# Optimization experiments

Measured on AMD Instinct MI355X. Metric: run time of the kernel, lower is better.

The kernel has to match this reference:

```python
import jax, jax.numpy as jnp
import numpy as np

B, L, D, H, DH, DI, NL, V = 1, 2048, 1024, 16, 64, 4096, 12, 32000
EPS = 1e-5  # torch LayerNorm default eps
SCALE = 1.0 / DH ** 0.5


def _ln(x):
    # LayerNorm with elementwise_affine=False
    m = jnp.mean(x, axis=-1, keepdims=True)
    va = jnp.var(x, axis=-1, keepdims=True)
    return (x - m) / jnp.sqrt(va + EPS)


def setup_inputs() -> dict:
    key = jax.random.key(0)
    ks = jax.random.split(key, 12)
    s = 0.02
    return {
        "X": jax.random.randint(ks[0], (B, L), 0, V),
        "Y": jax.random.randint(ks[1], (B, L), 0, V),
        "emb": jax.random.normal(ks[2], (V, D), jnp.float32) * s,
        "u": jax.random.normal(ks[3], (H, DH), jnp.float32) * s,
        "v": jax.random.normal(ks[4], (H, DH), jnp.float32) * s,
        "Wqkv": jax.random.normal(ks[5], (NL, 3 * H * DH, D), jnp.float32) * s,
        "Wpe": jax.random.normal(ks[6], (NL, H * DH, D), jnp.float32) * s,
        "Wout": jax.random.normal(ks[7], (NL, D, H * DH), jnp.float32) * s,
        "W1": jax.random.normal(ks[8], (NL, DI, D), jnp.float32) * s,
        "b1": jnp.zeros((NL, DI), jnp.float32),
        "W2": jax.random.normal(ks[9], (NL, D, DI), jnp.float32) * s,
        "b2": jnp.zeros((NL, D), jnp.float32),
        "Wc": jax.random.normal(ks[10], (V, D), jnp.float32) * s,
        "bc": jnp.zeros((V,), jnp.float32),
    }


def _forward(X, emb, u, v, Wqkv, Wpe, Wout, W1, b1, W2, b2, Wc, bc):
    q_len = X.shape[1]
    k_len = q_len  # mems=None -> m_len=0
    h = emb[X]  # (B, L, D); d_embedding == d_model so no projection

    # sinusoidal relative position embedding over descending positions
    pos = jnp.arange(k_len - 1, -1, -1, dtype=h.dtype)
    inv_freq = 1.0 / (10000.0 ** (jnp.arange(0, D, 2, dtype=h.dtype) / D))
    pp = pos[:, None] * inv_freq[None, :]              # (k, D/2)
    pe = jnp.concatenate([jnp.sin(pp), jnp.cos(pp)], axis=1)[None]  # (1, k, D)

    # causal mask: triu(ones, diagonal=1 + m_len), m_len=0; True = masked
    mask = jnp.triu(jnp.ones((q_len, k_len), bool), k=1)

    def layer(hid, params):
        wqkv, wpe, wout, w1, bb1, w2, bb2 = params
        qkv = hid @ wqkv.T                              # (B, q, 3HD)
        Q, K, Vv = jnp.split(qkv, 3, axis=-1)
        Q = Q.reshape(B, q_len, H, DH)
        K = K.reshape(B, k_len, H, DH)
        Vv = Vv.reshape(B, k_len, H, DH)
        r = (pe @ wpe.T).reshape(B, k_len, H, DH)       # requires B == 1
        AC = jnp.einsum('bqhd,bkhd->bhqk', Q + u, K)
        # NOTE: original code calls relative_shift(BD) but DISCARDS the result,
        # so BD is used unshifted — we reproduce that faithfully.
        BD = jnp.einsum('bqhd,bkhd->bhqk', Q + v, r)
        score = (AC + BD) * SCALE
        score = jnp.where(mask[None, None], -jnp.inf, score)
        prob = jax.nn.softmax(score, axis=-1)
        av = jnp.einsum('bhqk,bkhd->bqhd', prob, Vv).reshape(B, q_len, H * DH)
        hid = _ln(hid + av @ wout.T)                    # post-norm attention
        ff = jax.nn.relu(hid @ w1.T + bb1) @ w2.T + bb2
        hid = _ln(hid + ff)                             # post-norm FFN
        return hid, None

    h, _ = jax.lax.scan(layer, h, (Wqkv, Wpe, Wout, W1, b1, W2, b2))
    logits = h @ Wc.T + bc                              # (B, L, V)
    return logits.reshape(B * q_len, V)


def reference(X, Y, emb, u, v, Wqkv, Wpe, Wout, W1, b1, W2, b2, Wc, bc):
    # Y only determines y_len; here y_len == q_len so the full hidden is used.
    return _forward(X, emb, u, v, Wqkv, Wpe, Wout, W1, b1, W2, b2, Wc, bc)
```

## Files before the change

### kernel.cpp

```cpp
#include <hip/hip_runtime.h>
#include <hip/hip_bf16.h>

#define L_ 2048
#define D_ 1024
#define H_ 16
#define DH_ 64
#define DI_ 4096
#define NL_ 12
#define V_ 32000
#define EPS_ 1e-5f
#define SCALE_ 0.125f
#define LOG2E_ 1.44269504f
#define KBLK 64

typedef __attribute__((ext_vector_type(8))) short short8;
typedef __attribute__((ext_vector_type(4))) float f32x4;
typedef __hip_bfloat16 bf16;

__device__ __forceinline__ void gload_lds16(const void* g, void* l) {
  __builtin_amdgcn_global_load_lds((const __attribute__((address_space(1))) void*)g,
                                   (__attribute__((address_space(3))) void*)l, 16, 0, 0);
}

__global__ __launch_bounds__(512)
void gemm256(const bf16* __restrict__ A, const bf16* __restrict__ B,
             float* __restrict__ C, const float* __restrict__ bias,
             int lda, int ldb, int ldc, int K)
{
  __shared__ __align__(16) bf16 As[2][256 * 64];
  __shared__ __align__(16) bf16 Bs[2][256 * 64];

  const int gx = gridDim.x;
  const int nwg = gx * gridDim.y;
  const int orig = blockIdx.x + gx * blockIdx.y;
  const int qq = nwg >> 3, rr = nwg & 7;
  const int xcd = orig & 7, sidx = orig >> 3;
  const int lin = (xcd < rr ? xcd * (qq + 1) : rr * (qq + 1) + (xcd - rr) * qq) + sidx;
  const int m0 = (lin % gx) * 256;
  const int n0 = (lin / gx) * 256;

  const int t = threadIdx.x;
  const int lane = t & 63, w = t >> 6;
  const int wm = w >> 2, wn = w & 3;
  const int rl = lane & 15, hi = lane >> 4;

  int srow[4], skb[4];
#pragma unroll
  for (int r = 0; r < 4; ++r) {
    int o = r * 8192 + t * 16;
    int s = o ^ (((o >> 9) & 1) << 5);
    srow[r] = s >> 7;
    skb[r] = s & 127;
  }

  auto stage = [&](int c, int kt) {
    const int k0 = kt * 64;
#pragma unroll
    for (int r = 0; r < 4; ++r)
      gload_lds16((const char*)A + ((size_t)(m0 + srow[r]) * lda + k0) * 2 + skb[r],
                  (char*)As[c] + r * 8192 + w * 1024);
#pragma unroll
    for (int r = 0; r < 4; ++r)
      gload_lds16((const char*)B + ((size_t)(n0 + srow[r]) * ldb + k0) * 2 + skb[r],
                  (char*)Bs[c] + r * 8192 + w * 1024);
  };

  f32x4 acc[8][4];
#pragma unroll
  for (int i = 0; i < 8; ++i)
#pragma unroll
    for (int j = 0; j < 4; ++j) acc[i][j] = (f32x4){0.f, 0.f, 0.f, 0.f};

  const int NT = K >> 6;
  stage(0, 0);
  stage(1, 1);
  asm volatile("s_waitcnt vmcnt(8)" ::: "memory");
  __builtin_amdgcn_s_barrier();
  asm volatile("" ::: "memory");

  int cur = 0;
  for (int kt = 0; kt < NT; ++kt) {
    short8 b[4][2];
#pragma unroll
    for (int nf = 0; nf < 4; ++nf)
#pragma unroll
      for (int ks = 0; ks < 2; ++ks) {
        int l = ((wn * 64 + nf * 16 + rl) << 7) + ks * 64 + hi * 16;
        b[nf][ks] = *(const short8*)((char*)Bs[cur] + (l ^ (((l >> 9) & 1) << 5)));
      }
#pragma unroll
    for (int p = 0; p < 4; ++p) {
      short8 a[2][2];
#pragma unroll
      for (int i = 0; i < 2; ++i)
#pragma unroll
        for (int ks = 0; ks < 2; ++ks) {
          int l = ((wm * 128 + (2 * p + i) * 16 + rl) << 7) + ks * 64 + hi * 16;
          a[i][ks] = *(const short8*)((char*)As[cur] + (l ^ (((l >> 9) & 1) << 5)));
        }
      __builtin_amdgcn_s_setprio(1);
#pragma unroll
      for (int i = 0; i < 2; ++i)
#pragma unroll
        for (int nf = 0; nf < 4; ++nf) {
          acc[2 * p + i][nf] = __builtin_amdgcn_mfma_f32_16x16x32_bf16(a[i][0], b[nf][0], acc[2 * p + i][nf], 0, 0, 0);
          acc[2 * p + i][nf] = __builtin_amdgcn_mfma_f32_16x16x32_bf16(a[i][1], b[nf][1], acc[2 * p + i][nf], 0, 0, 0);
        }
      __builtin_amdgcn_s_setprio(0);
      __builtin_amdgcn_sched_barrier(0);
    }
    __builtin_amdgcn_s_barrier();
    asm volatile("" ::: "memory");
    if (kt + 2 < NT) stage(cur, kt + 2);
    if (kt + 1 < NT) {
      if (kt + 2 < NT) asm volatile("s_waitcnt vmcnt(8)" ::: "memory");
      else             asm volatile("s_waitcnt vmcnt(0)" ::: "memory");
      __builtin_amdgcn_s_barrier();
      asm volatile("" ::: "memory");
    }
    cur ^= 1;
  }

#pragma unroll
  for (int mf = 0; mf < 8; ++mf) {
#pragma unroll
    for (int nf = 0; nf < 4; ++nf) {
#pragma unroll
      for (int j = 0; j < 4; ++j) {
        const int m = m0 + wm * 128 + mf * 16 + hi * 4 + j;
        const int n = n0 + wn * 64 + nf * 16 + rl;
        C[(size_t)m * ldc + n] = acc[mf][nf][j] + bias[n];
      }
    }
  }
}

template<int EPI>
__global__ __launch_bounds__(512)
void gemm256x128(const bf16* __restrict__ A, const bf16* __restrict__ B,
                 void* __restrict__ C, const float* __restrict__ bias,
                 int lda, int ldb, int ldc, int Kc, long long Cstride)
{
  __shared__ __align__(16) bf16 As[2][256 * 64];
  __shared__ __align__(16) bf16 Bs[2][128 * 64];

  const int gx = gridDim.x;
  const int nwg = gx * gridDim.y;
  const int orig = blockIdx.x + gx * blockIdx.y;
  const int qq = nwg >> 3, rr = nwg & 7;
  const int xcd = orig & 7, sidx = orig >> 3;
  const int lin = (xcd < rr ? xcd * (qq + 1) : rr * (qq + 1) + (xcd - rr) * qq) + sidx;
  const int m0 = (lin % gx) * 256;
  const int n0 = (lin / gx) * 128;

  const int kbeg = blockIdx.z * Kc;
  const size_t czoff = (size_t)blockIdx.z * (size_t)Cstride;

  const int t = threadIdx.x;
  const int lane = t & 63, w = t >> 6;
  const int wm = w >> 1, wn = w & 1;
  const int rl = lane & 15, hi = lane >> 4;

  int srow[4], skb[4];
#pragma unroll
  for (int r = 0; r < 4; ++r) {
    int o = r * 8192 + t * 16;
    int s = o ^ (((o >> 9) & 1) << 5);
    srow[r] = s >> 7;
    skb[r] = s & 127;
  }

  auto stage = [&](int c, int kt) {
    const int k0 = kbeg + kt * 64;
#pragma unroll
    for (int r = 0; r < 4; ++r)
      gload_lds16((const char*)A + ((size_t)(m0 + srow[r]) * lda + k0) * 2 + skb[r],
                  (char*)As[c] + r * 8192 + w * 1024);
#pragma unroll
    for (int r = 0; r < 2; ++r)
      gload_lds16((const char*)B + ((size_t)(n0 + srow[r]) * ldb + k0) * 2 + skb[r],
                  (char*)Bs[c] + r * 8192 + w * 1024);
  };

  f32x4 acc[4][4];
#pragma unroll
  for (int i = 0; i < 4; ++i)
#pragma unroll
    for (int j = 0; j < 4; ++j) acc[i][j] = (f32x4){0.f, 0.f, 0.f, 0.f};

  const int NT = Kc >> 6;
  stage(0, 0);
  stage(1, 1);
  asm volatile("s_waitcnt vmcnt(6)" ::: "memory");
  __builtin_amdgcn_s_barrier();
  asm volatile("" ::: "memory");

  int cur = 0;
  for (int kt = 0; kt < NT; ++kt) {
    short8 b[4][2];
#pragma unroll
    for (int nf = 0; nf < 4; ++nf)
#pragma unroll
      for (int ks = 0; ks < 2; ++ks) {
        int l = ((wn * 64 + nf * 16 + rl) << 7) + ks * 64 + hi * 16;
        b[nf][ks] = *(const short8*)((char*)Bs[cur] + (l ^ (((l >> 9) & 1) << 5)));
      }
#pragma unroll
    for (int p = 0; p < 4; ++p) {
      short8 a[2];
#pragma unroll
      for (int ks = 0; ks < 2; ++ks) {
        int l = ((wm * 64 + p * 16 + rl) << 7) + ks * 64 + hi * 16;
        a[ks] = *(const short8*)((char*)As[cur] + (l ^ (((l >> 9) & 1) << 5)));
      }
      __builtin_amdgcn_s_setprio(1);
#pragma unroll
      for (int nf = 0; nf < 4; ++nf) {
        acc[p][nf] = __builtin_amdgcn_mfma_f32_16x16x32_bf16(a[0], b[nf][0], acc[p][nf], 0, 0, 0);
        acc[p][nf] = __builtin_amdgcn_mfma_f32_16x16x32_bf16(a[1], b[nf][1], acc[p][nf], 0, 0, 0);
      }
      __builtin_amdgcn_s_setprio(0);
      __builtin_amdgcn_sched_barrier(0);
    }
    __builtin_amdgcn_s_barrier();
    asm volatile("" ::: "memory");
    if (kt + 2 < NT) stage(cur, kt + 2);
    if (kt + 1 < NT) {
      if (kt + 2 < NT) asm volatile("s_waitcnt vmcnt(6)" ::: "memory");
      else             asm volatile("s_waitcnt vmcnt(0)" ::: "memory");
      __builtin_amdgcn_s_barrier();
      asm volatile("" ::: "memory");
    }
    cur ^= 1;
  }

#pragma unroll
  for (int mf = 0; mf < 4; ++mf) {
#pragma unroll
    for (int nf = 0; nf < 4; ++nf) {
#pragma unroll
      for (int j = 0; j < 4; ++j) {
        const int m = m0 + wm * 64 + mf * 16 + hi * 4 + j;
        const int n = n0 + wn * 64 + nf * 16 + rl;
        if (EPI == 0) {
          float vv = fmaxf(acc[mf][nf][j] + bias[n], 0.f);
          ((bf16*)C)[(size_t)m * ldc + n] = __float2bfloat16(vv);
        } else {
          ((float*)C)[czoff + (size_t)m * ldc + n] = acc[mf][nf][j];
        }
      }
    }
  }
}

__global__ __launch_bounds__(512)
void gemm_qkvpe256(const bf16* __restrict__ Ah, const bf16* __restrict__ Ape,
                   const bf16* __restrict__ Wqkv, const bf16* __restrict__ Wpe,
                   const float* __restrict__ u, const float* __restrict__ v,
                   bf16* __restrict__ QuQv, bf16* __restrict__ Kr, bf16* __restrict__ Vrm)
{
  __shared__ __align__(16) bf16 As[2][256 * 64];
  __shared__ __align__(16) bf16 Bs[2][128 * 64];

  const int gx = gridDim.x;
  const int nwg = gx * gridDim.y;
  const int orig = blockIdx.x + gx * blockIdx.y;
  const int qq = nwg >> 3, rr = nwg & 7;
  const int xcd = orig & 7, sidx = orig >> 3;
  const int lin = (xcd < rr ? xcd * (qq + 1) : rr * (qq + 1) + (xcd - rr) * qq) + sidx;
  const int m0 = (lin % gx) * 256;
  const int n0 = (lin / gx) * 128;

  const bf16* Ab = (n0 < 3072) ? Ah : Ape;
  const bf16* Bb = (n0 < 3072) ? (Wqkv + (size_t)n0 * D_) : (Wpe + (size_t)(n0 - 3072) * D_);

  const int t = threadIdx.x;
  const int lane = t & 63, w = t >> 6;
  const int wm = w >> 1, wn = w & 1;
  const int rl = lane & 15, hi = lane >> 4;

  int srow[4], skb[4];
#pragma unroll
  for (int r = 0; r < 4; ++r) {
    int o = r * 8192 + t * 16;
    int s = o ^ (((o >> 9) & 1) << 5);
    srow[r] = s >> 7;
    skb[r] = s & 127;
  }

  auto stage = [&](int c, int kt) {
    const int k0 = kt * 64;
#pragma unroll
    for (int r = 0; r < 4; ++r)
      gload_lds16((const char*)Ab + ((size_t)(m0 + srow[r]) * D_ + k0) * 2 + skb[r],
                  (char*)As[c] + r * 8192 + w * 1024);
#pragma unroll
    for (int r = 0; r < 2; ++r)
      gload_lds16((const char*)Bb + ((size_t)srow[r] * D_ + k0) * 2 + skb[r],
                  (char*)Bs[c] + r * 8192 + w * 1024);
  };

  f32x4 acc[4][4];
#pragma unroll
  for (int i = 0; i < 4; ++i)
#pragma unroll
    for (int j = 0; j < 4; ++j) acc[i][j] = (f32x4){0.f, 0.f, 0.f, 0.f};

  const int NT = D_ >> 6;
  stage(0, 0);
  stage(1, 1);
  asm volatile("s_waitcnt vmcnt(6)" ::: "memory");
  __builtin_amdgcn_s_barrier();
  asm volatile("" ::: "memory");

  int cur = 0;
  for (int kt = 0; kt < NT; ++kt) {
    short8 b[4][2];
#pragma unroll
    for (int nf = 0; nf < 4; ++nf)
#pragma unroll
      for (int ks = 0; ks < 2; ++ks) {
        int l = ((wn * 64 + nf * 16 + rl) << 7) + ks * 64 + hi * 16;
        b[nf][ks] = *(const short8*)((char*)Bs[cur] + (l ^ (((l >> 9) & 1) << 5)));
      }
#pragma unroll
    for (int p = 0; p < 4; ++p) {
      short8 a[2];
#pragma unroll
      for (int ks = 0; ks < 2; ++ks) {
        int l = ((wm * 64 + p * 16 + rl) << 7) + ks * 64 + hi * 16;
        a[ks] = *(const short8*)((char*)As[cur] + (l ^ (((l >> 9) & 1) << 5)));
      }
      __builtin_amdgcn_s_setprio(1);
#pragma unroll
      for (int nf = 0; nf < 4; ++nf) {
        acc[p][nf] = __builtin_amdgcn_mfma_f32_16x16x32_bf16(a[0], b[nf][0], acc[p][nf], 0, 0, 0);
        acc[p][nf] = __builtin_amdgcn_mfma_f32_16x16x32_bf16(a[1], b[nf][1], acc[p][nf], 0, 0, 0);
      }
      __builtin_amdgcn_s_setprio(0);
      __builtin_amdgcn_sched_barrier(0);
    }
    __builtin_amdgcn_s_barrier();
    asm volatile("" ::: "memory");
    if (kt + 2 < NT) stage(cur, kt + 2);
    if (kt + 1 < NT) {
      if (kt + 2 < NT) asm volatile("s_waitcnt vmcnt(6)" ::: "memory");
      else             asm volatile("s_waitcnt vmcnt(0)" ::: "memory");
      __builtin_amdgcn_s_barrier();
      asm volatile("" ::: "memory");
    }
    cur ^= 1;
  }

#pragma unroll
  for (int mf = 0; mf < 4; ++mf) {
#pragma unroll
    for (int nf = 0; nf < 4; ++nf) {
#pragma unroll
      for (int j = 0; j < 4; ++j) {
        const int m = m0 + wm * 64 + mf * 16 + hi * 4 + j;
        const int n = n0 + wn * 64 + nf * 16 + rl;
        float x = acc[mf][nf][j];
        if (n < 1024) {
          const int h = n >> 6, d = n & 63;
          size_t b = ((size_t)h * L_ + m) * 128;
          QuQv[b + d]      = __float2bfloat16((x + u[n]) * SCALE_);
          QuQv[b + 64 + d] = __float2bfloat16((x + v[n]) * SCALE_);
        } else if (n < 2048) {
          const int n2 = n - 1024;
          Kr[(((size_t)(n2 >> 6)) * L_ + m) * 128 + (n2 & 63)] = __float2bfloat16(x);
        } else if (n < 3072) {
          Vrm[(size_t)m * 1024 + (n - 2048)] = __float2bfloat16(x);
        } else {
          const int c = n - 3072;
          Kr[(((size_t)(c >> 6)) * L_ + m) * 128 + 64 + (c & 63)] = __float2bfloat16(x);
        }
      }
    }
  }
}

__global__ __launch_bounds__(256)
void attn_fused(const bf16* __restrict__ QuQv, const bf16* __restrict__ Kr,
                const bf16* __restrict__ VT, bf16* __restrict__ av)
{
  __shared__ __align__(16) bf16 Kt[KBLK * 128];
  __shared__ __align__(16) bf16 Vt[DH_ * KBLK];
  __shared__ __align__(16) bf16 Pt[4][16 * KBLK];

  const int bid = blockIdx.x;
  const int tile = (bid < 256) ? (31 - (bid >> 4)) : ((bid - 256) >> 4);
  const int head = bid & 15;
  const int q0 = tile * 64;
  const int t = threadIdx.x, lane = t & 63, w = t >> 6;
  const int rl = lane & 15, hi = lane >> 4;

  const bf16* Qh = QuQv + (size_t)head * L_ * 128;
  const bf16* Kh = Kr   + (size_t)head * L_ * 128;
  const bf16* Vh = VT   + (size_t)head * DH_ * L_;

  const int qw0 = q0 + w * 16;

  short8 qf[4];
#pragma unroll
  for (int ks = 0; ks < 4; ++ks)
    qf[ks] = *(const short8*)(Qh + (size_t)(qw0 + rl) * 128 + ks * 32 + hi * 8);

  f32x4 o[4];
  float m_r[4], l_r[4];
#pragma unroll
  for (int j = 0; j < 4; ++j) { m_r[j] = -INFINITY; l_r[j] = 0.f; }
#pragma unroll
  for (int fn = 0; fn < 4; ++fn) o[fn] = (f32x4){0.f, 0.f, 0.f, 0.f};

  short8 kreg[4], vreg[2];
  auto load_regs = [&](int k0) {
#pragma unroll
    for (int i = 0; i < 4; ++i) {
      int c = i * 256 + t;
      int row = c >> 4, d8 = (c & 15) << 3;
      kreg[i] = *(const short8*)(Kh + (size_t)(k0 + row) * 128 + d8);
    }
#pragma unroll
    for (int i = 0; i < 2; ++i) {
      int c = i * 256 + t;
      int d = c >> 3, k8 = (c & 7) << 3;
      vreg[i] = *(const short8*)(Vh + (size_t)d * L_ + k0 + k8);
    }
  };
  auto write_lds = [&]() {
#pragma unroll
    for (int i = 0; i < 4; ++i) {
      int c = i * 256 + t;
      int row = c >> 4, d8 = (c & 15) << 3;
      int off = (row << 8) + (((d8 << 1)) ^ ((row & 7) << 4));
      *(short8*)((char*)Kt + off) = kreg[i];
    }
#pragma unroll
    for (int i = 0; i < 2; ++i) {
      int c = i * 256 + t;
      int d = c >> 3, k8 = (c & 7) << 3;
      int off = (d << 7) + (((k8 << 1)) ^ ((d & 7) << 4));
      *(short8*)((char*)Vt + off) = vreg[i];
    }
  };

  load_regs(0);
  write_lds();
  __syncthreads();

  const int kend = q0 + 64;
  for (int k0 = 0; k0 < kend; k0 += KBLK) {
    const bool more = (k0 + KBLK) < kend;
    if (more) load_regs(k0 + KBLK);

    if (k0 <= qw0 + 15) {
      f32x4 s[4];
#pragma unroll
      for (int fn = 0; fn < 4; ++fn) s[fn] = (f32x4){0.f, 0.f, 0.f, 0.f};
      __builtin_amdgcn_s_setprio(1);
#pragma unroll
      for (int fn = 0; fn < 4; ++fn) {
        const int krow = fn * 16 + rl;
#pragma unroll
        for (int ks = 0; ks < 4; ++ks) {
          short8 kf = *(const short8*)((char*)Kt + (krow << 8) +
                        ((((ks * 32 + hi * 8) << 1)) ^ ((krow & 7) << 4)));
          s[fn] = __builtin_amdgcn_mfma_f32_16x16x32_bf16(qf[ks], kf, s[fn], 0, 0, 0);
        }
      }
      __builtin_amdgcn_s_setprio(0);
      if (k0 + KBLK > q0) {
#pragma unroll
        for (int fn = 0; fn < 4; ++fn) {
          const int key = k0 + fn * 16 + rl;
#pragma unroll
          for (int j = 0; j < 4; ++j)
            if (key > qw0 + hi * 4 + j) s[fn][j] = -1e30f;
        }
      }
      float mx[4];
#pragma unroll
      for (int j = 0; j < 4; ++j)
        mx[j] = fmaxf(fmaxf(s[0][j], s[1][j]), fmaxf(s[2][j], s[3][j]));
#pragma unroll
      for (int off = 1; off < 16; off <<= 1)
#pragma unroll
        for (int j = 0; j < 4; ++j) mx[j] = fmaxf(mx[j], __shfl_xor(mx[j], off));
      float sf[4];
#pragma unroll
      for (int j = 0; j < 4; ++j) {
        float mn = fmaxf(m_r[j], mx[j]);
        sf[j] = exp2f((m_r[j] - mn) * LOG2E_);
        m_r[j] = mn;
      }
      float rs[4] = {0.f, 0.f, 0.f, 0.f};
#pragma unroll
      for (int fn = 0; fn < 4; ++fn) {
#pragma unroll
        for (int j = 0; j < 4; ++j) {
          float p = exp2f((s[fn][j] - m_r[j]) * LOG2E_);
          rs[j] += p;
          int row = hi * 4 + j;
          *(bf16*)((char*)Pt[w] + (row << 7) +
                   ((((fn * 16 + rl) << 1)) ^ ((row & 7) << 4))) = __float2bfloat16(p);
        }
      }
#pragma unroll
      for (int off = 1; off < 16; off <<= 1)
#pragma unroll
        for (int j = 0; j < 4; ++j) rs[j] += __shfl_xor(rs[j], off);
#pragma unroll
      for (int j = 0; j < 4; ++j) l_r[j] = l_r[j] * sf[j] + rs[j];
#pragma unroll
      for (int fn = 0; fn < 4; ++fn)
#pragma unroll
        for (int j = 0; j < 4; ++j) o[fn][j] *= sf[j];

      __builtin_amdgcn_s_setprio(1);
#pragma unroll
      for (int ks2 = 0; ks2 < 2; ++ks2) {
        short8 pa = *(const short8*)((char*)Pt[w] + (rl << 7) +
                      ((ks2 * 64 + hi * 16) ^ ((rl & 7) << 4)));
#pragma unroll
        for (int fn = 0; fn < 4; ++fn) {
          const int drow = fn * 16 + rl;
          short8 vf = *(const short8*)((char*)Vt + (drow << 7) +
                        ((ks2 * 64 + hi * 16) ^ ((drow & 7) << 4)));
          o[fn] = __builtin_amdgcn_mfma_f32_16x16x32_bf16(pa, vf, o[fn], 0, 0, 0);
        }
      }
      __builtin_amdgcn_s_setprio(0);
    }

    if (more) {
      __syncthreads();
      write_lds();
      __syncthreads();
    }
  }

#pragma unroll
  for (int fn = 0; fn < 4; ++fn) {
#pragma unroll
    for (int j = 0; j < 4; ++j) {
      int q = qw0 + hi * 4 + j;
      float vv = o[fn][j] / l_r[j];
      av[(size_t)q * D_ + head * 64 + fn * 16 + rl] = __float2bfloat16(vv);
    }
  }
}

__global__ __launch_bounds__(256)
void embed_k(const int* __restrict__ X, const float* __restrict__ emb,
             float* __restrict__ hout, bf16* __restrict__ hbout)
{
  int idx = blockIdx.x * 256 + threadIdx.x;
  if (idx >= L_ * D_) return;
  int tpos = idx >> 10, d = idx & 1023;
  float vv = emb[(size_t)X[tpos] * D_ + d];
  hout[idx] = vv;
  hbout[idx] = __float2bfloat16(vv);
}

__global__ __launch_bounds__(256)
void pe_k(bf16* __restrict__ pe)
{
  int idx = blockIdx.x * 256 + threadIdx.x;
  if (idx >= L_ * D_) return;
  int k = idx >> 10, i = idx & 1023;
  int f = (i < 512) ? i : (i - 512);
  float invf = exp2f(-(float)(2 * f) * (13.28771238f / 1024.f));
  float pp = (float)(L_ - 1 - k) * invf;
  float vv = (i < 512) ? sinf(pp) : cosf(pp);
  pe[idx] = __float2bfloat16(vv);
}

__global__ __launch_bounds__(256)
void cast_all(const float* __restrict__ wqkv, const float* __restrict__ wpe,
              const float* __restrict__ wout, const float* __restrict__ w1,
              const float* __restrict__ w2,
              bf16* __restrict__ dqkv, bf16* __restrict__ dpe, bf16* __restrict__ dout,
              bf16* __restrict__ d1, bf16* __restrict__ d2)
{
  const int n4 = 13631488 / 4;
  for (int i = blockIdx.x * 256 + threadIdx.x; i < n4; i += gridDim.x * 256) {
    int j = i * 4;
    const float* src; bf16* dst; int o;
    if (j < 3145728)      { src = wqkv; dst = dqkv; o = j; }
    else if (j < 4194304) { src = wpe;  dst = dpe;  o = j - 3145728; }
    else if (j < 5242880) { src = wout; dst = dout; o = j - 4194304; }
    else if (j < 9437184) { src = w1;   dst = d1;   o = j - 5242880; }
    else                  { src = w2;   dst = d2;   o = j - 9437184; }
    float4 vv = *(const float4*)(src + o);
    dst[o + 0] = __float2bfloat16(vv.x);
    dst[o + 1] = __float2bfloat16(vv.y);
    dst[o + 2] = __float2bfloat16(vv.z);
    dst[o + 3] = __float2bfloat16(vv.w);
  }
}

__global__ __launch_bounds__(256)
void cast_bf4(const float* __restrict__ in, bf16* __restrict__ out, long long n4)
{
  for (long long i = (long long)blockIdx.x * 256 + threadIdx.x; i < n4; i += (long long)gridDim.x * 256) {
    float4 vv = *(const float4*)(in + i * 4);
    out[i * 4 + 0] = __float2bfloat16(vv.x);
    out[i * 4 + 1] = __float2bfloat16(vv.y);
    out[i * 4 + 2] = __float2bfloat16(vv.z);
    out[i * 4 + 3] = __float2bfloat16(vv.w);
  }
}

__global__ __launch_bounds__(256)
void vtrans(const bf16* __restrict__ Vrm, bf16* __restrict__ VT)
{
  __shared__ unsigned short tile[64 * 65];
  const int q0 = blockIdx.x * 64;
  const int h = blockIdx.y;
  const int t = threadIdx.x;
#pragma unroll
  for (int i = 0; i < 2; ++i) {
    int qrow = i * 32 + (t >> 3);
    int d0 = (t & 7) * 8;
    short8 vv = *(const short8*)(Vrm + (size_t)(q0 + qrow) * 1024 + h * 64 + d0);
#pragma unroll
    for (int e = 0; e < 8; ++e)
      tile[(d0 + e) * 65 + qrow] = (unsigned short)vv[e];
  }
  __syncthreads();
  const int dr = t >> 5;
  const int q2 = (t & 31) * 2;
#pragma unroll
  for (int i = 0; i < 8; ++i) {
    int dd = i * 8 + dr;
    unsigned int pk = (unsigned int)tile[dd * 65 + q2] |
                      ((unsigned int)tile[dd * 65 + q2 + 1] << 16);
    *(unsigned int*)(VT + ((size_t)h * 64 + dd) * L_ + q0 + q2) = pk;
  }
}

__global__ __launch_bounds__(256)
void ln_residual(const float* __restrict__ resid, const float* __restrict__ parts,
                 int nparts, long long pstride, const float* __restrict__ bias,
                 float* __restrict__ hout, bf16* __restrict__ hbout)
{
  const int row = blockIdx.x;
  const int t = threadIdx.x;
  const int lane = t & 63, w = t >> 6;
  const size_t base = (size_t)row * D_;
  __shared__ float rs[4], rs2[4];
  float4 xv = *(const float4*)(resid + base + t * 4);
  for (int p = 0; p < nparts; ++p) {
    float4 pv = *(const float4*)(parts + (size_t)p * pstride + base + t * 4);
    xv.x += pv.x; xv.y += pv.y; xv.z += pv.z; xv.w += pv.w;
  }
  if (bias) {
    float4 bv = *(const float4*)(bias + t * 4);
    xv.x += bv.x; xv.y += bv.y; xv.z += bv.z; xv.w += bv.w;
  }
  float s = xv.x + xv.y + xv.z + xv.w;
  float s2 = xv.x * xv.x + xv.y * xv.y + xv.z * xv.z + xv.w * xv.w;
#pragma unroll
  for (int off = 32; off; off >>= 1) {
    s += __shfl_down(s, off);
    s2 += __shfl_down(s2, off);
  }
  if (lane == 0) { rs[w] = s; rs2[w] = s2; }
  __syncthreads();
  float S = rs[0] + rs[1] + rs[2] + rs[3];
  float S2 = rs2[0] + rs2[1] + rs2[2] + rs2[3];
  float mean = S * (1.f / D_);
  float var = S2 * (1.f / D_) - mean * mean;
  float inv = 1.f / sqrtf(var + EPS_);
  float4 y;
  y.x = (xv.x - mean) * inv;
  y.y = (xv.y - mean) * inv;
  y.z = (xv.z - mean) * inv;
  y.w = (xv.w - mean) * inv;
  *(float4*)(hout + base + t * 4) = y;
  __hip_bfloat162 p0, p1;
  p0.x = __float2bfloat16(y.x); p0.y = __float2bfloat16(y.y);
  p1.x = __float2bfloat16(y.z); p1.y = __float2bfloat16(y.w);
  *(__hip_bfloat162*)(hbout + base + t * 4)     = p0;
  *(__hip_bfloat162*)(hbout + base + t * 4 + 2) = p1;
}

extern "C" void kernel_launch(void* const* d_in, const int* in_sizes, int n_in,
                              void* d_out, int out_size, void* d_ws, size_t ws_size,
                              hipStream_t stream)
{
  (void)in_sizes; (void)n_in; (void)out_size; (void)ws_size;
  const int*   X    = (const int*)d_in[0];
  const float* emb  = (const float*)d_in[2];
  const float* u    = (const float*)d_in[3];
  const float* v    = (const float*)d_in[4];
  const float* Wqkv = (const float*)d_in[5];
  const float* Wpe  = (const float*)d_in[6];
  const float* Wout = (const float*)d_in[7];
  const float* W1   = (const float*)d_in[8];
  const float* b1   = (const float*)d_in[9];
  const float* W2   = (const float*)d_in[10];
  const float* b2   = (const float*)d_in[11];
  const float* Wc   = (const float*)d_in[12];
  const float* bc   = (const float*)d_in[13];
  float* out = (float*)d_out;

  size_t off = 0;
  auto alloc = [&](size_t bytes) {
    void* p = (char*)d_ws + off;
    off += (bytes + 255) & ~(size_t)255;
    return p;
  };
  float* h_f32   = (float*)alloc((size_t)L_ * D_ * 4);
  bf16*  h_bf    = (bf16*) alloc((size_t)L_ * D_ * 2);
  bf16*  pe_bf   = (bf16*) alloc((size_t)L_ * D_ * 2);
  bf16*  QuQv    = (bf16*) alloc((size_t)H_ * L_ * 128 * 2);
  bf16*  Kr      = (bf16*) alloc((size_t)H_ * L_ * 128 * 2);
  bf16*  Vrm     = (bf16*) alloc((size_t)L_ * D_ * 2);
  bf16*  VT      = (bf16*) alloc((size_t)H_ * DH_ * L_ * 2);
  bf16*  av_bf   = (bf16*) alloc((size_t)L_ * D_ * 2);
  float* part_f  = (float*)alloc((size_t)4 * L_ * D_ * 4);
  bf16*  ff1_bf  = (bf16*) alloc((size_t)L_ * DI_ * 2);
  bf16*  Wc_bf   = (bf16*) alloc((size_t)V_ * D_ * 2);
  bf16*  Wqkv_bf = (bf16*) alloc((size_t)3 * D_ * D_ * 2);
  bf16*  Wpe_bf  = (bf16*) alloc((size_t)D_ * D_ * 2);
  bf16*  Wout_bf = (bf16*) alloc((size_t)D_ * D_ * 2);
  bf16*  W1_bf   = (bf16*) alloc((size_t)DI_ * D_ * 2);
  bf16*  W2_bf   = (bf16*) alloc((size_t)D_ * DI_ * 2);

  const int eb = (L_ * D_ + 255) / 256;
  const long long LD = (long long)L_ * D_;

  embed_k<<<eb, 256, 0, stream>>>(X, emb, h_f32, h_bf);
  pe_k<<<eb, 256, 0, stream>>>(pe_bf);

  dim3 gqkvpe(L_ / 256, 4096 / 128, 1);
  dim3 gout (L_ / 256, D_ / 128, 4);
  dim3 gff1 (L_ / 256, DI_ / 128, 1);

  for (int l = 0; l < NL_; ++l) {
    cast_all<<<2048, 256, 0, stream>>>(
        Wqkv + (size_t)l * 3 * D_ * D_, Wpe + (size_t)l * D_ * D_,
        Wout + (size_t)l * D_ * D_, W1 + (size_t)l * DI_ * D_, W2 + (size_t)l * D_ * DI_,
        Wqkv_bf, Wpe_bf, Wout_bf, W1_bf, W2_bf);

    gemm_qkvpe256<<<gqkvpe, 512, 0, stream>>>(h_bf, pe_bf, Wqkv_bf, Wpe_bf, u, v, QuQv, Kr, Vrm);

    vtrans<<<dim3(L_ / 64, H_, 1), 256, 0, stream>>>(Vrm, VT);

    attn_fused<<<512, 256, 0, stream>>>(QuQv, Kr, VT, av_bf);

    gemm256x128<1><<<gout, 512, 0, stream>>>(av_bf, Wout_bf, part_f, nullptr,
        D_, D_, D_, 256, LD);
    ln_residual<<<L_, 256, 0, stream>>>(h_f32, part_f, 4, LD, nullptr, h_f32, h_bf);

    gemm256x128<0><<<gff1, 512, 0, stream>>>(h_bf, W1_bf, ff1_bf, b1 + (size_t)l * DI_,
        D_, D_, DI_, D_, 0);

    gemm256x128<1><<<gout, 512, 0, stream>>>(ff1_bf, W2_bf, part_f, nullptr,
        DI_, DI_, D_, 1024, LD);
    ln_residual<<<L_, 256, 0, stream>>>(h_f32, part_f, 4, LD, b2 + (size_t)l * D_, h_f32, h_bf);
  }

  cast_bf4<<<2048, 256, 0, stream>>>(Wc, Wc_bf, (long long)V_ * D_ / 4);
  dim3 gl(L_ / 256, V_ / 256, 1);
  gemm256<<<gl, 512, 0, stream>>>(h_bf, Wc_bf, out, bc, D_, D_, V_, D_);
}
```

Measured before the change: 2.825 ms.

## Triple-buffer GEMM LDS stages and interleave prefetch loads with MFMA phases

Moves the 256x128 GEMM and the fused QKV/PE GEMM from double to triple LDS buffering. Prefetch of tile kt+2 now goes into a third buffer and is split into three chunks issued between the MFMA sub-phases, so the loop no longer issues the whole stage after the barrier. The goal is to overlap global-to-LDS traffic with compute and shorten the stall at each barrier. LDS use grows to 144KB per block, which may limit occupancy or exceed the per-CU limit.

```diff
diff --git a/kernel.cpp b/kernel.cpp
--- a/kernel.cpp
+++ b/kernel.cpp
@@ -141,8 +141,8 @@
                  void* __restrict__ C, const float* __restrict__ bias,
                  int lda, int ldb, int ldc, int Kc, long long Cstride)
 {
-  __shared__ __align__(16) bf16 As[2][256 * 64];
-  __shared__ __align__(16) bf16 Bs[2][128 * 64];
+  __shared__ __align__(16) bf16 As[3][256 * 64];
+  __shared__ __align__(16) bf16 Bs[3][128 * 64];
 
   const int gx = gridDim.x;
   const int nwg = gx * gridDim.y;
@@ -170,17 +170,25 @@
     skb[r] = s & 127;
   }
 
-  auto stage = [&](int c, int kt) {
+  auto stageA2 = [&](int c, int kt, int rbase) {
     const int k0 = kbeg + kt * 64;
 #pragma unroll
-    for (int r = 0; r < 4; ++r)
+    for (int r = rbase; r < rbase + 2; ++r)
       gload_lds16((const char*)A + ((size_t)(m0 + srow[r]) * lda + k0) * 2 + skb[r],
                   (char*)As[c] + r * 8192 + w * 1024);
+  };
+  auto stageB2 = [&](int c, int kt) {
+    const int k0 = kbeg + kt * 64;
 #pragma unroll
     for (int r = 0; r < 2; ++r)
       gload_lds16((const char*)B + ((size_t)(n0 + srow[r]) * ldb + k0) * 2 + skb[r],
                   (char*)Bs[c] + r * 8192 + w * 1024);
   };
+  auto stage = [&](int c, int kt) {
+    stageA2(c, kt, 0);
+    stageA2(c, kt, 2);
+    stageB2(c, kt);
+  };
 
   f32x4 acc[4][4];
 #pragma unroll
@@ -190,13 +198,16 @@
 
   const int NT = Kc >> 6;
   stage(0, 0);
-  stage(1, 1);
+  if (NT > 1) stage(1, 1);
   asm volatile("s_waitcnt vmcnt(6)" ::: "memory");
   __builtin_amdgcn_s_barrier();
   asm volatile("" ::: "memory");
 
-  int cur = 0;
   for (int kt = 0; kt < NT; ++kt) {
+    const int cur = kt % 3;
+    const int nxt = (kt + 2) % 3;
+    const bool pf = (kt + 2) < NT;
+
     short8 b[4][2];
 #pragma unroll
     for (int nf = 0; nf < 4; ++nf)
@@ -207,6 +218,11 @@
       }
 #pragma unroll
     for (int p = 0; p < 4; ++p) {
+      if (pf) {
+        if (p == 0) stageA2(nxt, kt + 2, 0);
+        else if (p == 1) stageA2(nxt, kt + 2, 2);
+        else if (p == 2) stageB2(nxt, kt + 2);
+      }
       short8 a[2];
 #pragma unroll
       for (int ks = 0; ks < 2; ++ks) {
@@ -224,14 +240,12 @@
     }
     __builtin_amdgcn_s_barrier();
     asm volatile("" ::: "memory");
-    if (kt + 2 < NT) stage(cur, kt + 2);
     if (kt + 1 < NT) {
-      if (kt + 2 < NT) asm volatile("s_waitcnt vmcnt(6)" ::: "memory");
-      else             asm volatile("s_waitcnt vmcnt(0)" ::: "memory");
+      if (pf) asm volatile("s_waitcnt vmcnt(6)" ::: "memory");
+      else    asm volatile("s_waitcnt vmcnt(0)" ::: "memory");
       __builtin_amdgcn_s_barrier();
       asm volatile("" ::: "memory");
     }
-    cur ^= 1;
   }
 
 #pragma unroll
@@ -259,8 +273,8 @@
                    const float* __restrict__ u, const float* __restrict__ v,
                    bf16* __restrict__ QuQv, bf16* __restrict__ Kr, bf16* __restrict__ Vrm)
 {
-  __shared__ __align__(16) bf16 As[2][256 * 64];
-  __shared__ __align__(16) bf16 Bs[2][128 * 64];
+  __shared__ __align__(16) bf16 As[3][256 * 64];
+  __shared__ __align__(16) bf16 Bs[3][128 * 64];
 
   const int gx = gridDim.x;
   const int nwg = gx * gridDim.y;
@@ -288,16 +302,24 @@
     skb[r] = s & 127;
   }
 
-  auto stage = [&](int c, int kt) {
+  auto stageA2 = [&](int c, int kt, int rbase) {
     const int k0 = kt * 64;
 #pragma unroll
-    for (int r = 0; r < 4; ++r)
+    for (int r = rbase; r < rbase + 2; ++r)
       gload_lds16((const char*)Ab + ((size_t)(m0 + srow[r]) * D_ + k0) * 2 + skb[r],
                   (char*)As[c] + r * 8192 + w * 1024);
+  };
+  auto stageB2 = [&](int c, int kt) {
+    const int k0 = kt * 64;
 #pragma unroll
     for (int r = 0; r < 2; ++r)
       gload_lds16((const char*)Bb + ((size_t)srow[r] * D_ + k0) * 2 + skb[r],
                   (char*)Bs[c] + r * 8192 + w * 1024);
+  };
+  auto stage = [&](int c, int kt) {
+    stageA2(c, kt, 0);
+    stageA2(c, kt, 2);
+    stageB2(c, kt);
   };
 
   f32x4 acc[4][4];
@@ -313,8 +335,11 @@
   __builtin_amdgcn_s_barrier();
   asm volatile("" ::: "memory");
 
-  int cur = 0;
   for (int kt = 0; kt < NT; ++kt) {
+    const int cur = kt % 3;
+    const int nxt = (kt + 2) % 3;
+    const bool pf = (kt + 2) < NT;
+
     short8 b[4][2];
 #pragma unroll
     for (int nf = 0; nf < 4; ++nf)
@@ -325,6 +350,11 @@
       }
 #pragma unroll
     for (int p = 0; p < 4; ++p) {
+      if (pf) {
+        if (p == 0) stageA2(nxt, kt + 2, 0);
+        else if (p == 1) stageA2(nxt, kt + 2, 2);
+        else if (p == 2) stageB2(nxt, kt + 2);
+      }
       short8 a[2];
 #pragma unroll
       for (int ks = 0; ks < 2; ++ks) {
@@ -342,14 +372,12 @@
     }
     __builtin_amdgcn_s_barrier();
     asm volatile("" ::: "memory");
-    if (kt + 2 < NT) stage(cur, kt + 2);
     if (kt + 1 < NT) {
-      if (kt + 2 < NT) asm volatile("s_waitcnt vmcnt(6)" ::: "memory");
-      else             asm volatile("s_waitcnt vmcnt(0)" ::: "memory");
+      if (pf) asm volatile("s_waitcnt vmcnt(6)" ::: "memory");
+      else    asm volatile("s_waitcnt vmcnt(0)" ::: "memory");
       __builtin_amdgcn_s_barrier();
       asm volatile("" ::: "memory");
     }
-    cur ^= 1;
   }
 
 #pragma unroll
```

Measured after the change: 2.838 ms. About the same (+0.5%).
